# Optimization experiments

Measured on AMD Instinct MI355X. Metric: run time of the kernel, lower is better.

The kernel has to match this reference:

```python
import jax, jax.numpy as jnp
import numpy as np


def _min_dist(src, tgt):
    # Euclidean cdist via the |a|^2 + |b|^2 - 2ab expansion (same math as torch.cdist p=2),
    # then row-wise min/argmin. src: (S,3), tgt: (T,3) -> (S,), (S,)
    d2 = (
        jnp.sum(src * src, axis=1)[:, None]
        + jnp.sum(tgt * tgt, axis=1)[None, :]
        - 2.0 * (src @ tgt.T)
    )
    d = jnp.sqrt(jnp.maximum(d2, 0.0))
    return jnp.min(d, axis=1), jnp.argmin(d, axis=1)


def setup_inputs() -> dict:
    key = jax.random.key(0)
    k1, k2, k3 = jax.random.split(key, 3)
    N, M = 32768, 8192
    P = jax.random.normal(k1, (N, 3), dtype=jnp.float32)
    Ps = jax.random.normal(k2, (M, 3), dtype=jnp.float32)
    probabilities = jax.random.uniform(k3, (M,), dtype=jnp.float32)
    return {"P": P, "Ps": Ps, "probabilities": probabilities}


def reference(P, Ps, probabilities):
    # sampled -> original: min distance per sampled point
    dist_s_to_o, _ = _min_dist(Ps, P)
    # original -> sampled: min distance + index of nearest sampled point
    dist_o_to_s, min_indices = _min_dist(P, Ps)
    weighted_s_to_o = dist_s_to_o * probabilities
    weighted_o_to_s = dist_o_to_s * probabilities[min_indices]
    return weighted_s_to_o.sum() + weighted_o_to_s.sum()
```

## Files before the change

### kernel.cpp

```cpp
#include <hip/hip_runtime.h>
#include <math.h>

static constexpr int BLK = 256;
static constexpr int CH = 2048;
static constexpr int SUB = 256;
static constexpr int QB = 128;

typedef _Float16 f16x8 __attribute__((ext_vector_type(8)));
typedef float f32x16 __attribute__((ext_vector_type(16)));

__device__ __forceinline__ unsigned f2u(float f) { return __float_as_uint(f); }
__device__ __forceinline__ float u2f(unsigned u) { return __uint_as_float(u); }
__device__ __forceinline__ unsigned pk(_Float16 a, _Float16 b) {
    union { _Float16 h[2]; unsigned u; } c; c.h[0] = a; c.h[1] = b; return c.u;
}
union B128 { uint4 u; f16x8 h; };

__global__ void prep_kernel(unsigned long long* __restrict__ o2s,
                            unsigned* __restrict__ s2o,
                            float* __restrict__ out, int N, int M) {
    int i = blockIdx.x * blockDim.x + threadIdx.x;
    if (i < N) o2s[i] = ~0ull;
    if (i < M) s2o[i] = 0xFFFFFFFFu;
    if (i == 0) out[0] = 0.0f;
}

__global__ void __launch_bounds__(BLK)
__attribute__((amdgpu_waves_per_eu(4, 4))) main_kernel(
    const float* __restrict__ P, const float* __restrict__ Ps,
    unsigned long long* __restrict__ o2s, unsigned* __restrict__ s2o,
    int N, int M, int o2sBlocks, int o2sRG, int s2oRG) {
    __shared__ uint4 lds16[SUB + 1];
    int tid = threadIdx.x;
    int lane = tid & 63, wave = tid >> 6;
    int n = lane & 31, half = lane >> 5;
    if (tid == 0) lds16[SUB] = make_uint4(0u, 0u, 0u, 0u);

    int bx = blockIdx.x;
    bool isO2S = bx < o2sBlocks;
    const float* qsrc; const float* ssrc;
    int i0, j0, scnt;
    if (isO2S) {
        int rg = bx % o2sRG, c = bx / o2sRG;
        i0 = rg * QB + wave * 32; j0 = c * CH; scnt = M;
        qsrc = P; ssrc = Ps;
    } else {
        int b = bx - o2sBlocks;
        int rg = b % s2oRG, c = b / s2oRG;
        i0 = rg * QB + wave * 32; j0 = c * CH; scnt = N;
        qsrc = Ps; ssrc = P;
    }

    f16x8 af;
    {
        float x = 0.f, y = 0.f, z = 0.f;
        if (half == 0) {
            int i = i0 + n;
            x = qsrc[3 * i]; y = qsrc[3 * i + 1]; z = qsrc[3 * i + 2];
        }
        _Float16 hx = (_Float16)x, hy = (_Float16)y, hz = (_Float16)z;
        _Float16 one = (half == 0) ? (_Float16)1.0f : (_Float16)0.0f;
        af = (f16x8){(_Float16)-hx, (_Float16)-hy, (_Float16)-hz, one,
                     (_Float16)0.0f, (_Float16)0.0f, (_Float16)0.0f, (_Float16)0.0f};
    }

    float runm[16];
#pragma unroll
    for (int r = 0; r < 16; ++r) runm[r] = __builtin_inff();
    f32x16 zacc = {};

    for (int s = 0; s < CH / SUB; ++s) {
        __syncthreads();
        {
            int jj = j0 + s * SUB + tid;
            jj = min(jj, scnt - 1);
            float x = ssrc[3 * jj], y = ssrc[3 * jj + 1], z = ssrc[3 * jj + 2];
            _Float16 hx = (_Float16)x, hy = (_Float16)y, hz = (_Float16)z;
            float fx = (float)hx, fy = (float)hy, fz = (float)hz;
            _Float16 hw = (_Float16)(0.5f * (fx * fx + fy * fy + fz * fz));
            lds16[tid] = make_uint4(pk(hx, hy), pk(hz, hw), 0u, 0u);
        }
        __syncthreads();
        float smin[16];
#pragma unroll
        for (int r = 0; r < 16; ++r) smin[r] = __builtin_inff();
#pragma unroll
        for (int t = 0; t < SUB / 32; t += 4) {
            B128 b0, b1, b2, b3;
            b0.u = lds16[half ? SUB : ((t + 0) * 32 + n)];
            b1.u = lds16[half ? SUB : ((t + 1) * 32 + n)];
            b2.u = lds16[half ? SUB : ((t + 2) * 32 + n)];
            b3.u = lds16[half ? SUB : ((t + 3) * 32 + n)];
            f32x16 c0 = __builtin_amdgcn_mfma_f32_32x32x16_f16(af, b0.h, zacc, 0, 0, 0);
            f32x16 c1 = __builtin_amdgcn_mfma_f32_32x32x16_f16(af, b1.h, zacc, 0, 0, 0);
            f32x16 c2 = __builtin_amdgcn_mfma_f32_32x32x16_f16(af, b2.h, zacc, 0, 0, 0);
            f32x16 c3 = __builtin_amdgcn_mfma_f32_32x32x16_f16(af, b3.h, zacc, 0, 0, 0);
#pragma unroll
            for (int r = 0; r < 16; ++r) {
                smin[r] = fminf(fminf(smin[r], c0[r]), c1[r]);
                smin[r] = fminf(fminf(smin[r], c2[r]), c3[r]);
            }
        }
        if (isO2S) {
#pragma unroll
            for (int r = 0; r < 16; ++r)
                runm[r] = fminf(runm[r], u2f((f2u(smin[r]) & ~0xFFu) | (unsigned)s));
        } else {
#pragma unroll
            for (int r = 0; r < 16; ++r)
                runm[r] = fminf(runm[r], smin[r]);
        }
    }

    if (isO2S) {
#pragma unroll
        for (int r = 0; r < 16; ++r) {
            unsigned u = f2u(runm[r]);
            runm[r] = u2f((u & ~0xFFu) | ((u & 7u) << 5) | (unsigned)n);
        }
    }
#pragma unroll
    for (int mask = 1; mask < 32; mask <<= 1) {
#pragma unroll
        for (int r = 0; r < 16; ++r)
            runm[r] = fminf(runm[r], __shfl_xor(runm[r], mask, 64));
    }
    if (n < 16) {
        int r = n;
        int row = (r & 3) + 8 * (r >> 2) + 4 * half;
        int i = i0 + row;
        float x = qsrc[3 * i], y = qsrc[3 * i + 1], z = qsrc[3 * i + 2];
        _Float16 hx = (_Float16)x, hy = (_Float16)y, hz = (_Float16)z;
        float fx = (float)hx, fy = (float)hy, fz = (float)hz;
        float nx = -fx, ny = -fy, nz = -fz;
        float pw = 0.5f * (fx * fx + fy * fy + fz * fz);
        if (isO2S) {
            unsigned uv = f2u(runm[r]);
            int sWin = (int)((uv >> 5) & 7u);
            int col = (int)(uv & 31u);
            float best = __builtin_inff();
            int bj = 0;
#pragma unroll
            for (int t = 0; t < 8; ++t) {
                int j = j0 + sWin * SUB + t * 32 + col;
                float sx = (float)(_Float16)ssrc[3 * j];
                float sy = (float)(_Float16)ssrc[3 * j + 1];
                float sz = (float)(_Float16)ssrc[3 * j + 2];
                float sw = 0.5f * (sx * sx + sy * sy + sz * sz);
                float m = fmaf(sx, nx, fmaf(sy, ny, fmaf(sz, nz, sw)));
                if (m < best) { best = m; bj = j; }
            }
            float d2 = fmaxf(2.0f * (pw + best), 0.0f);
            unsigned long long key =
                ((unsigned long long)f2u(d2) << 32) | (unsigned)bj;
            atomicMin(&o2s[i], key);
        } else {
            float d2 = fmaxf(2.0f * (pw + runm[r]), 0.0f);
            atomicMin(&s2o[i], f2u(d2));
        }
    }
}

__global__ void finish_kernel(const unsigned* __restrict__ s2o,
                              const unsigned long long* __restrict__ o2s,
                              const float* __restrict__ prob,
                              float* __restrict__ out, int N, int M) {
    int t = blockIdx.x * BLK + threadIdx.x;
    float acc = 0.0f;
    if (t < M) {
        acc = sqrtf(u2f(s2o[t])) * prob[t];
    } else if (t < M + N) {
        unsigned long long key = o2s[t - M];
        float d2 = u2f((unsigned)(key >> 32));
        unsigned jj = (unsigned)(key & 0xFFFFFFFFu);
        acc = sqrtf(d2) * prob[jj];
    }
#pragma unroll
    for (int off = 32; off > 0; off >>= 1) acc += __shfl_down(acc, off, 64);
    __shared__ float wsum[BLK / 64];
    int lane = threadIdx.x & 63, wave = threadIdx.x >> 6;
    if (lane == 0) wsum[wave] = acc;
    __syncthreads();
    if (threadIdx.x == 0) {
        float s = 0.0f;
#pragma unroll
        for (int w = 0; w < BLK / 64; ++w) s += wsum[w];
        atomicAdd(out, s);
    }
}

extern "C" void kernel_launch(void* const* d_in, const int* in_sizes, int n_in,
                              void* d_out, int out_size, void* d_ws, size_t ws_size,
                              hipStream_t stream) {
    const float* P = (const float*)d_in[0];
    const float* Ps = (const float*)d_in[1];
    const float* prob = (const float*)d_in[2];
    int N = in_sizes[0] / 3;
    int M = in_sizes[1] / 3;
    float* out = (float*)d_out;

    unsigned long long* o2s = (unsigned long long*)d_ws;
    unsigned* s2o = (unsigned*)((char*)d_ws + (size_t)N * 8);

    int o2sRG = N / QB;
    int s2oRG = M / QB;
    int o2sBlocks = o2sRG * (M / CH);
    int s2oBlocks = s2oRG * (N / CH);
    int total = o2sBlocks + s2oBlocks;

    prep_kernel<<<(N + BLK - 1) / BLK, BLK, 0, stream>>>(o2s, s2o, out, N, M);
    main_kernel<<<total, BLK, 0, stream>>>(P, Ps, o2s, s2o, N, M,
                                           o2sBlocks, o2sRG, s2oRG);
    finish_kernel<<<(N + M + BLK - 1) / BLK, BLK, 0, stream>>>(s2o, o2s, prob,
                                                               out, N, M);
}
```

Measured before the change: 91.96 us.

## Prepack fp16 points in prep kernel and stage whole chunk in LDS once

The prep kernel now converts P and Ps once into packed fp16 (x,y,z,0.5|p|^2) records in workspace. The main kernel loads its entire 2048-point chunk into LDS with vectorized 16-byte loads and a single barrier, replacing the per-256-point loads, conversions and two barriers per sub-iteration. B operands are built in registers with zero upper halves instead of reading a zero LDS slot for the upper half-wave. This cuts redundant conversion work and synchronization, at the cost of more LDS per block (16KB) and extra workspace traffic in prep.

After: 89.98 us. 2.2% less time.

```diff
diff --git a/kernel.cpp b/kernel.cpp
--- a/kernel.cpp
+++ b/kernel.cpp
@@ -14,54 +14,84 @@
 __device__ __forceinline__ unsigned pk(_Float16 a, _Float16 b) {
     union { _Float16 h[2]; unsigned u; } c; c.h[0] = a; c.h[1] = b; return c.u;
 }
-union B128 { uint4 u; f16x8 h; };
-
-__global__ void prep_kernel(unsigned long long* __restrict__ o2s,
+
+__device__ __forceinline__ f16x8 mk_b(uint2 v) {
+    union { unsigned u[4]; f16x8 h; } c;
+    c.u[0] = v.x; c.u[1] = v.y; c.u[2] = 0u; c.u[3] = 0u;
+    return c.h;
+}
+
+__global__ void prep_kernel(const float* __restrict__ P,
+                            const float* __restrict__ Ps,
+                            unsigned long long* __restrict__ o2s,
                             unsigned* __restrict__ s2o,
+                            uint2* __restrict__ pkP, uint2* __restrict__ pkPs,
                             float* __restrict__ out, int N, int M) {
     int i = blockIdx.x * blockDim.x + threadIdx.x;
-    if (i < N) o2s[i] = ~0ull;
-    if (i < M) s2o[i] = 0xFFFFFFFFu;
+    if (i < N) {
+        o2s[i] = ~0ull;
+        float x = P[3 * i], y = P[3 * i + 1], z = P[3 * i + 2];
+        _Float16 hx = (_Float16)x, hy = (_Float16)y, hz = (_Float16)z;
+        float fx = (float)hx, fy = (float)hy, fz = (float)hz;
+        _Float16 hw = (_Float16)(0.5f * (fx * fx + fy * fy + fz * fz));
+        pkP[i] = make_uint2(pk(hx, hy), pk(hz, hw));
+    }
+    if (i < M) {
+        s2o[i] = 0xFFFFFFFFu;
+        float x = Ps[3 * i], y = Ps[3 * i + 1], z = Ps[3 * i + 2];
+        _Float16 hx = (_Float16)x, hy = (_Float16)y, hz = (_Float16)z;
+        float fx = (float)hx, fy = (float)hy, fz = (float)hz;
+        _Float16 hw = (_Float16)(0.5f * (fx * fx + fy * fy + fz * fz));
+        pkPs[i] = make_uint2(pk(hx, hy), pk(hz, hw));
+    }
     if (i == 0) out[0] = 0.0f;
 }
 
 __global__ void __launch_bounds__(BLK)
 __attribute__((amdgpu_waves_per_eu(4, 4))) main_kernel(
     const float* __restrict__ P, const float* __restrict__ Ps,
+    const uint2* __restrict__ pkP, const uint2* __restrict__ pkPs,
     unsigned long long* __restrict__ o2s, unsigned* __restrict__ s2o,
     int N, int M, int o2sBlocks, int o2sRG, int s2oRG) {
-    __shared__ uint4 lds16[SUB + 1];
+    __shared__ uint2 lds2[CH];
     int tid = threadIdx.x;
     int lane = tid & 63, wave = tid >> 6;
     int n = lane & 31, half = lane >> 5;
-    if (tid == 0) lds16[SUB] = make_uint4(0u, 0u, 0u, 0u);
 
     int bx = blockIdx.x;
     bool isO2S = bx < o2sBlocks;
     const float* qsrc; const float* ssrc;
-    int i0, j0, scnt;
+    const uint2* pkq; const uint2* pks;
+    int i0, j0;
     if (isO2S) {
         int rg = bx % o2sRG, c = bx / o2sRG;
-        i0 = rg * QB + wave * 32; j0 = c * CH; scnt = M;
-        qsrc = P; ssrc = Ps;
+        i0 = rg * QB + wave * 32; j0 = c * CH;
+        qsrc = P; ssrc = Ps; pkq = pkP; pks = pkPs;
     } else {
         int b = bx - o2sBlocks;
         int rg = b % s2oRG, c = b / s2oRG;
-        i0 = rg * QB + wave * 32; j0 = c * CH; scnt = N;
-        qsrc = Ps; ssrc = P;
+        i0 = rg * QB + wave * 32; j0 = c * CH;
+        qsrc = Ps; ssrc = P; pkq = pkPs; pks = pkP;
+    }
+
+    {
+        const uint4* g4 = (const uint4*)pks + (j0 >> 1);
+        uint4* l4 = (uint4*)lds2;
+#pragma unroll
+        for (int k = 0; k < 4; ++k) l4[k * BLK + tid] = g4[k * BLK + tid];
     }
 
     f16x8 af;
     {
-        float x = 0.f, y = 0.f, z = 0.f;
+        unsigned d0 = 0u, d1 = 0u;
         if (half == 0) {
-            int i = i0 + n;
-            x = qsrc[3 * i]; y = qsrc[3 * i + 1]; z = qsrc[3 * i + 2];
-        }
-        _Float16 hx = (_Float16)x, hy = (_Float16)y, hz = (_Float16)z;
-        _Float16 one = (half == 0) ? (_Float16)1.0f : (_Float16)0.0f;
-        af = (f16x8){(_Float16)-hx, (_Float16)-hy, (_Float16)-hz, one,
-                     (_Float16)0.0f, (_Float16)0.0f, (_Float16)0.0f, (_Float16)0.0f};
+            uint2 q = pkq[i0 + n];
+            d0 = q.x ^ 0x80008000u;
+            d1 = ((q.y ^ 0x00008000u) & 0x0000FFFFu) | 0x3C000000u;
+        }
+        union { unsigned u[4]; f16x8 h; } a;
+        a.u[0] = d0; a.u[1] = d1; a.u[2] = 0u; a.u[3] = 0u;
+        af = a.h;
     }
 
     float runm[16];
@@ -69,32 +99,23 @@
     for (int r = 0; r < 16; ++r) runm[r] = __builtin_inff();
     f32x16 zacc = {};
 
+    __syncthreads();
+
     for (int s = 0; s < CH / SUB; ++s) {
-        __syncthreads();
-        {
-            int jj = j0 + s * SUB + tid;
-            jj = min(jj, scnt - 1);
-            float x = ssrc[3 * jj], y = ssrc[3 * jj + 1], z = ssrc[3 * jj + 2];
-            _Float16 hx = (_Float16)x, hy = (_Float16)y, hz = (_Float16)z;
-            float fx = (float)hx, fy = (float)hy, fz = (float)hz;
-            _Float16 hw = (_Float16)(0.5f * (fx * fx + fy * fy + fz * fz));
-            lds16[tid] = make_uint4(pk(hx, hy), pk(hz, hw), 0u, 0u);
-        }
-        __syncthreads();
         float smin[16];
 #pragma unroll
         for (int r = 0; r < 16; ++r) smin[r] = __builtin_inff();
 #pragma unroll
         for (int t = 0; t < SUB / 32; t += 4) {
-            B128 b0, b1, b2, b3;
-            b0.u = lds16[half ? SUB : ((t + 0) * 32 + n)];
-            b1.u = lds16[half ? SUB : ((t + 1) * 32 + n)];
-            b2.u = lds16[half ? SUB : ((t + 2) * 32 + n)];
-            b3.u = lds16[half ? SUB : ((t + 3) * 32 + n)];
-            f32x16 c0 = __builtin_amdgcn_mfma_f32_32x32x16_f16(af, b0.h, zacc, 0, 0, 0);
-            f32x16 c1 = __builtin_amdgcn_mfma_f32_32x32x16_f16(af, b1.h, zacc, 0, 0, 0);
-            f32x16 c2 = __builtin_amdgcn_mfma_f32_32x32x16_f16(af, b2.h, zacc, 0, 0, 0);
-            f32x16 c3 = __builtin_amdgcn_mfma_f32_32x32x16_f16(af, b3.h, zacc, 0, 0, 0);
+            int base = s * SUB + t * 32 + n;
+            uint2 v0 = lds2[base];
+            uint2 v1 = lds2[base + 32];
+            uint2 v2 = lds2[base + 64];
+            uint2 v3 = lds2[base + 96];
+            f32x16 c0 = __builtin_amdgcn_mfma_f32_32x32x16_f16(af, mk_b(v0), zacc, 0, 0, 0);
+            f32x16 c1 = __builtin_amdgcn_mfma_f32_32x32x16_f16(af, mk_b(v1), zacc, 0, 0, 0);
+            f32x16 c2 = __builtin_amdgcn_mfma_f32_32x32x16_f16(af, mk_b(v2), zacc, 0, 0, 0);
+            f32x16 c3 = __builtin_amdgcn_mfma_f32_32x32x16_f16(af, mk_b(v3), zacc, 0, 0, 0);
 #pragma unroll
             for (int r = 0; r < 16; ++r) {
                 smin[r] = fminf(fminf(smin[r], c0[r]), c1[r]);
@@ -199,8 +220,11 @@
     int M = in_sizes[1] / 3;
     float* out = (float*)d_out;
 
-    unsigned long long* o2s = (unsigned long long*)d_ws;
-    unsigned* s2o = (unsigned*)((char*)d_ws + (size_t)N * 8);
+    char* ws = (char*)d_ws;
+    unsigned long long* o2s = (unsigned long long*)ws;
+    unsigned* s2o = (unsigned*)(ws + (size_t)N * 8);
+    uint2* pkP = (uint2*)(ws + (size_t)N * 8 + (size_t)M * 4);
+    uint2* pkPs = (uint2*)(ws + (size_t)N * 16 + (size_t)M * 4);
 
     int o2sRG = N / QB;
     int s2oRG = M / QB;
@@ -208,8 +232,9 @@
     int s2oBlocks = s2oRG * (N / CH);
     int total = o2sBlocks + s2oBlocks;
 
-    prep_kernel<<<(N + BLK - 1) / BLK, BLK, 0, stream>>>(o2s, s2o, out, N, M);
-    main_kernel<<<total, BLK, 0, stream>>>(P, Ps, o2s, s2o, N, M,
+    prep_kernel<<<(N + BLK - 1) / BLK, BLK, 0, stream>>>(P, Ps, o2s, s2o,
+                                                         pkP, pkPs, out, N, M);
+    main_kernel<<<total, BLK, 0, stream>>>(P, Ps, pkP, pkPs, o2s, s2o, N, M,
                                            o2sBlocks, o2sRG, s2oRG);
     finish_kernel<<<(N + M + BLK - 1) / BLK, BLK, 0, stream>>>(s2o, o2s, prob,
                                                                out, N, M);
```
